# Optimization experiments

Measured on AMD Instinct MI355X. Metric: run time of the kernel, lower is better.

The kernel has to match this reference:

```python
import jax, jax.numpy as jnp
import numpy as np
from jax.scipy.stats import norm

N_TOK, D_MODEL, N_EXP, N_SEL = 16384, 4096, 16, 4
NOISE_EPS = 0.01
LOSS_LAMBDA = 0.01


def setup_inputs() -> dict:
    key = jax.random.key(0)
    kx, k1, k2, kn, kz = jax.random.split(key, 5)
    x = jax.random.normal(kx, (N_TOK, D_MODEL), dtype=jnp.float32)
    w1 = jax.random.normal(k1, (N_EXP, D_MODEL), dtype=jnp.float32) * 0.02
    w2 = jax.random.normal(k2, (N_EXP, N_EXP), dtype=jnp.float32) * 0.02
    wn = jax.random.normal(kn, (N_EXP, D_MODEL), dtype=jnp.float32) * 0.02
    noise = jax.random.normal(kz, (N_TOK, N_EXP), dtype=jnp.float32)
    return {"x": x, "w1": w1, "w2": w2, "wn": wn, "noise": noise}


def _cv_squared(v, eps=1e-10):
    # torch .var() is unbiased (ddof=1)
    return jnp.var(v, ddof=1) / (jnp.mean(v) ** 2 + eps)


def reference(x, w1, w2, wn, noise):
    # MLP gate: Linear(D->E, no bias) -> tanh -> Linear(E->E, no bias)
    logits_gate = jnp.einsum("te,fe->tf", jnp.tanh(jnp.einsum("td,ed->te", x, w1)), w2)
    noise_control = jax.nn.softplus(jnp.einsum("td,ed->te", x, wn)) + NOISE_EPS
    logits_noise = noise * noise_control
    logits = logits_gate + logits_noise  # [T, E]

    m = min(N_SEL + 1, N_EXP)  # k+1 values for threshold computation
    top_logits, top_indices = jax.lax.top_k(logits, m)  # [T, m]
    top_k_logits = top_logits[:, :N_SEL]
    top_k_indices = top_indices[:, :N_SEL]
    top_k_scores = jax.nn.softmax(top_k_logits, axis=1)  # [T, k]

    # importance: scatter top-k scores back to dense [T, E]
    rows = jnp.arange(N_TOK)[:, None]
    scores_filtered = jnp.zeros_like(logits).at[rows, top_k_indices].set(top_k_scores)
    importance = scores_filtered.sum(0)  # [E]

    # load: smooth estimator via Normal CDF (faithful to source, which
    # compares logits_noise against the in/out thresholds)
    threshold_if_in = top_logits[:, N_SEL:N_SEL + 1]       # (k+1)-th top value, [T,1]
    threshold_if_out = top_logits[:, N_SEL - 1:N_SEL]      # k-th top value, [T,1]
    is_in = logits_noise > threshold_if_in
    prob_if_in = norm.cdf((logits_gate - threshold_if_in) / noise_control)
    prob_if_out = norm.cdf((logits_gate - threshold_if_out) / noise_control)
    prob = jnp.where(is_in, prob_if_in, prob_if_out)
    load = prob.sum(0)  # [E]

    gate_loss = LOSS_LAMBDA * (_cv_squared(importance) + _cv_squared(load))
    return top_k_indices, top_k_scores, gate_loss
```

## Files before the change

### kernel.cpp

```cpp
#include <hip/hip_runtime.h>
#include <math.h>

#define N_TOK   16384
#define D_MODEL 4096
#define N_EXP   16
#define N_SEL   4
#define WELEM   (N_EXP * D_MODEL)
#define TILES   4

typedef __bf16 bf16x8 __attribute__((ext_vector_type(8)));
typedef float  f32x4  __attribute__((ext_vector_type(4)));

#define MFMA(a, b, c) __builtin_amdgcn_mfma_f32_16x16x32_bf16((a), (b), (c), 0, 0, 0)

__global__ __launch_bounds__(256) void wprep_kernel(const float* __restrict__ w1,
                                                    const float* __restrict__ wn,
                                                    __bf16* __restrict__ wbuf,
                                                    float* __restrict__ g_acc)
{
    const int i = blockIdx.x * 256 + threadIdx.x;
    if (blockIdx.x == 0 && threadIdx.x < 2 * N_EXP) g_acc[threadIdx.x] = 0.f;
    {
        const float v = w1[i];
        const __bf16 h = (__bf16)v;  const float r1 = v - (float)h;
        const __bf16 m = (__bf16)r1; const float r2 = r1 - (float)m;
        wbuf[i] = h; wbuf[WELEM + i] = m; wbuf[2 * WELEM + i] = (__bf16)r2;
    }
    {
        const float v = wn[i];
        const __bf16 h = (__bf16)v;  const float r1 = v - (float)h;
        const __bf16 m = (__bf16)r1; const float r2 = r1 - (float)m;
        wbuf[3 * WELEM + i] = h; wbuf[4 * WELEM + i] = m; wbuf[5 * WELEM + i] = (__bf16)r2;
    }
}

__device__ __forceinline__ void split8(const float4 a, const float4 b,
                                       bf16x8& h, bf16x8& m, bf16x8& l)
{
    const float v[8] = {a.x, a.y, a.z, a.w, b.x, b.y, b.z, b.w};
    #pragma unroll
    for (int j = 0; j < 8; ++j) {
        const float vv = v[j];
        const __bf16 hh = (__bf16)vv;  const float r1 = vv - (float)hh;
        const __bf16 mm = (__bf16)r1;  const float r2 = r1 - (float)mm;
        h[j] = hh; m[j] = mm; l[j] = (__bf16)r2;
    }
}

__global__ __launch_bounds__(512, 4) void gate_kernel(
    const float* __restrict__ x, const __bf16* __restrict__ wbuf,
    const float* __restrict__ w2, const float* __restrict__ noise,
    float* __restrict__ out, float* __restrict__ g_imp, float* __restrict__ g_load)
{
    __shared__ float red[8][TILES][16][33];
    __shared__ float dsum[TILES][16][33];
    __shared__ float s_imp[N_EXP], s_ld[N_EXP];

    const int tid  = threadIdx.x;
    const int lane = tid & 63;
    const int wv   = tid >> 6;
    const int ml   = lane & 15;
    const int q    = lane >> 4;
    const int t0   = blockIdx.x * (TILES * 16);

    const __bf16* w1h = wbuf;
    const __bf16* w1m = wbuf + WELEM;
    const __bf16* w1l = wbuf + 2 * WELEM;
    const __bf16* wnh = wbuf + 3 * WELEM;
    const __bf16* wnm = wbuf + 4 * WELEM;
    const __bf16* wnl = wbuf + 5 * WELEM;

    const size_t xoff0 = (size_t)(t0 + ml) * D_MODEL + wv * 512 + q * 8;
    const int    woff  = ml * D_MODEL + wv * 512 + q * 8;

    f32x4 c1[TILES], c2[TILES];
    #pragma unroll
    for (int tt = 0; tt < TILES; ++tt) {
        c1[tt] = (f32x4){0.f, 0.f, 0.f, 0.f};
        c2[tt] = (f32x4){0.f, 0.f, 0.f, 0.f};
    }

    #pragma unroll 2
    for (int it = 0; it < 16; ++it) {
        const int ko = it * 32;
        const bf16x8 a1h = *(const bf16x8*)(w1h + woff + ko);
        const bf16x8 a1m = *(const bf16x8*)(w1m + woff + ko);
        const bf16x8 a1l = *(const bf16x8*)(w1l + woff + ko);
        const bf16x8 a2h = *(const bf16x8*)(wnh + woff + ko);
        const bf16x8 a2m = *(const bf16x8*)(wnm + woff + ko);
        const bf16x8 a2l = *(const bf16x8*)(wnl + woff + ko);
        float4 xa[TILES], xb[TILES];
        #pragma unroll
        for (int tt = 0; tt < TILES; ++tt) {
            const size_t xo = xoff0 + (size_t)(16 * tt) * D_MODEL + ko;
            xa[tt] = *(const float4*)(x + xo);
            xb[tt] = *(const float4*)(x + xo + 4);
        }

        #pragma unroll
        for (int tt = 0; tt < TILES; ++tt) {
            bf16x8 xh, xm8, xl;
            split8(xa[tt], xb[tt], xh, xm8, xl);
            c1[tt] = MFMA(a1h, xh, c1[tt]);   c2[tt] = MFMA(a2h, xh, c2[tt]);
            c1[tt] = MFMA(a1h, xm8, c1[tt]);  c2[tt] = MFMA(a2h, xm8, c2[tt]);
            c1[tt] = MFMA(a1m, xh, c1[tt]);   c2[tt] = MFMA(a2m, xh, c2[tt]);
            c1[tt] = MFMA(a1h, xl, c1[tt]);   c2[tt] = MFMA(a2h, xl, c2[tt]);
            c1[tt] = MFMA(a1l, xh, c1[tt]);   c2[tt] = MFMA(a2l, xh, c2[tt]);
            c1[tt] = MFMA(a1m, xm8, c1[tt]);  c2[tt] = MFMA(a2m, xm8, c2[tt]);
        }
    }

    #pragma unroll
    for (int tt = 0; tt < TILES; ++tt) {
        #pragma unroll
        for (int r = 0; r < 4; ++r) {
            red[wv][tt][ml][q * 4 + r]      = c1[tt][r];
            red[wv][tt][ml][16 + q * 4 + r] = c2[tt][r];
        }
    }
    __syncthreads();

    for (int idx = tid; idx < TILES * 512; idx += 512) {
        const int tt = idx >> 9, tk = (idx >> 5) & 15, o = idx & 31;
        float s = 0.f;
        #pragma unroll
        for (int w = 0; w < 8; ++w) s += red[w][tt][tk][o];
        dsum[tt][tk][o] = s;
    }
    if (tid < N_EXP) { s_imp[tid] = 0.f; s_ld[tid] = 0.f; }
    __syncthreads();

    if (tid < TILES * 16) {
        const int tt = tid >> 4, tk = tid & 15;
        const int t = t0 + tid;
        float dot[32];
        #pragma unroll
        for (int e = 0; e < 32; ++e) dot[e] = dsum[tt][tk][e];

        float th[N_EXP], nc[N_EXP];
        #pragma unroll
        for (int e = 0; e < N_EXP; ++e) th[e] = tanhf(dot[e]);
        #pragma unroll
        for (int e = 0; e < N_EXP; ++e) {
            const float v = dot[N_EXP + e];
            nc[e] = fmaxf(v, 0.f) + log1pf(expf(-fabsf(v))) + 0.01f;
        }

        float lg[N_EXP];
        #pragma unroll
        for (int f = 0; f < N_EXP; ++f) {
            float s = 0.f;
            #pragma unroll
            for (int e = 0; e < N_EXP; ++e) s = fmaf(th[e], w2[f * 16 + e], s);
            lg[f] = s;
        }

        float ln[N_EXP], v[N_EXP];
        {
            const float4* nz = (const float4*)(noise + (size_t)t * 16);
            const float4 n0 = nz[0], n1 = nz[1], n2 = nz[2], n3 = nz[3];
            const float nzv[16] = {n0.x, n0.y, n0.z, n0.w, n1.x, n1.y, n1.z, n1.w,
                                   n2.x, n2.y, n2.z, n2.w, n3.x, n3.y, n3.z, n3.w};
            #pragma unroll
            for (int e = 0; e < N_EXP; ++e) {
                ln[e] = nzv[e] * nc[e];
                v[e]  = lg[e] + ln[e];
            }
        }

        float tv[5]; int ti[5];
        #pragma unroll
        for (int j = 0; j < 5; ++j) {
            float best = -INFINITY; int bi = 0;
            #pragma unroll
            for (int e = 0; e < N_EXP; ++e) {
                bool taken = false;
                #pragma unroll
                for (int jj = 0; jj < 5; ++jj)
                    if (jj < j) taken = taken || (ti[jj] == e);
                if (!taken && v[e] > best) { best = v[e]; bi = e; }
            }
            tv[j] = best; ti[j] = bi;
        }

        const float mx = tv[0];
        float ex[4], ssum = 0.f;
        #pragma unroll
        for (int j = 0; j < 4; ++j) { ex[j] = expf(tv[j] - mx); ssum += ex[j]; }
        const float inv = 1.f / ssum;
        float sc[4];
        #pragma unroll
        for (int j = 0; j < 4; ++j) sc[j] = ex[j] * inv;

        #pragma unroll
        for (int j = 0; j < 4; ++j) atomicAdd(&s_imp[ti[j]], sc[j]);

        const float thr_in = tv[4], thr_out = tv[3];
        #pragma unroll
        for (int e = 0; e < N_EXP; ++e) {
            const bool  is_in = ln[e] > thr_in;
            const float thr   = is_in ? thr_in : thr_out;
            const float z     = (lg[e] - thr) / nc[e];
            const float prob  = 0.5f * (1.f + erff(z * 0.70710678118654752f));
            atomicAdd(&s_ld[e], prob);
        }

        ((float4*)out)[t] = make_float4((float)ti[0], (float)ti[1],
                                        (float)ti[2], (float)ti[3]);
        ((float4*)(out + N_TOK * N_SEL))[t] = make_float4(sc[0], sc[1], sc[2], sc[3]);
    }
    __syncthreads();
    if (tid < N_EXP)            atomicAdd(&g_imp[tid], s_imp[tid]);
    else if (tid < 2 * N_EXP)   atomicAdd(&g_load[tid - N_EXP], s_ld[tid - N_EXP]);
}

__global__ void loss_kernel(const float* __restrict__ g_imp,
                            const float* __restrict__ g_load,
                            float* __restrict__ out)
{
    if (threadIdx.x == 0 && blockIdx.x == 0) {
        double mi = 0.0, ml = 0.0;
        for (int e = 0; e < N_EXP; ++e) { mi += g_imp[e]; ml += g_load[e]; }
        mi /= N_EXP; ml /= N_EXP;
        double vi = 0.0, vl = 0.0;
        for (int e = 0; e < N_EXP; ++e) {
            const double di = g_imp[e] - mi;  vi += di * di;
            const double dl = g_load[e] - ml; vl += dl * dl;
        }
        vi /= (N_EXP - 1); vl /= (N_EXP - 1);
        const double ci = vi / (mi * mi + 1e-10);
        const double cl = vl / (ml * ml + 1e-10);
        out[N_TOK * N_SEL * 2] = (float)(0.01 * (ci + cl));
    }
}

extern "C" void kernel_launch(void* const* d_in, const int* in_sizes, int n_in,
                              void* d_out, int out_size, void* d_ws, size_t ws_size,
                              hipStream_t stream)
{
    const float* x     = (const float*)d_in[0];
    const float* w1    = (const float*)d_in[1];
    const float* w2    = (const float*)d_in[2];
    const float* wn    = (const float*)d_in[3];
    const float* noise = (const float*)d_in[4];
    float* out = (float*)d_out;

    __bf16* wbuf  = (__bf16*)d_ws;
    float*  g_imp = (float*)((char*)d_ws + (1 << 20));
    float*  g_load = g_imp + N_EXP;

    wprep_kernel<<<WELEM / 256, 256, 0, stream>>>(w1, wn, wbuf, g_imp);
    gate_kernel<<<N_TOK / (TILES * 16), 512, 0, stream>>>(x, wbuf, w2, noise, out,
                                                          g_imp, g_load);
    loss_kernel<<<1, 64, 0, stream>>>(g_imp, g_load, out);
}
```

Baseline: 415.7 us.

## Stage x tiles through double-buffered LDS with coalesced loads, halve tokens per block

Token tiles per block drop from 4 to 2 (32 tokens per block, twice as many blocks). Each K step now loads x with fully coalesced float4 global reads into one of two LDS buffers, prefetching the next step while MFMAs run on the current one. This is meant to fix the strided per-lane global access pattern and overlap memory latency with compute. It adds a __syncthreads per step and LDS traffic, and the smaller tile means the weight splits are reloaded per fewer tokens.

```diff
diff --git a/kernel.cpp b/kernel.cpp
--- a/kernel.cpp
+++ b/kernel.cpp
@@ -6,7 +6,7 @@
 #define N_EXP   16
 #define N_SEL   4
 #define WELEM   (N_EXP * D_MODEL)
-#define TILES   4
+#define TILES   2
 
 typedef __bf16 bf16x8 __attribute__((ext_vector_type(8)));
 typedef float  f32x4  __attribute__((ext_vector_type(4)));
@@ -52,8 +52,7 @@
     const float* __restrict__ w2, const float* __restrict__ noise,
     float* __restrict__ out, float* __restrict__ g_imp, float* __restrict__ g_load)
 {
-    __shared__ float red[8][TILES][16][33];
-    __shared__ float dsum[TILES][16][33];
+    __shared__ float smem[2][8 * 32 * 33];
     __shared__ float s_imp[N_EXP], s_ld[N_EXP];
 
     const int tid  = threadIdx.x;
@@ -70,8 +69,23 @@
     const __bf16* wnm = wbuf + 4 * WELEM;
     const __bf16* wnl = wbuf + 5 * WELEM;
 
-    const size_t xoff0 = (size_t)(t0 + ml) * D_MODEL + wv * 512 + q * 8;
-    const int    woff  = ml * D_MODEL + wv * 512 + q * 8;
+    const int woff = ml * D_MODEL + wv * 512 + q * 8;
+
+    int gb0, gb1, gb2, gb3, lb0, lb1, lb2, lb3;
+    {
+#define MAP(P, GB, LB)                                           \
+        {   const int fid  = (P) * 512 + tid;                    \
+            const int slot = fid & 7;                            \
+            const int s    = fid >> 3;                           \
+            const int r    = s >> 5;                             \
+            const int t    = s & 31;                             \
+            GB = (t0 + t) * D_MODEL + r * 512 + slot * 4;        \
+            LB = (r * 32 + t) * 33 + slot * 4;  }
+        MAP(0, gb0, lb0) MAP(1, gb1, lb1) MAP(2, gb2, lb2) MAP(3, gb3, lb3)
+#undef MAP
+    }
+    const int lr0 = (wv * 32 + ml) * 33 + q * 8;
+    const int lr1 = lr0 + 16 * 33;
 
     f32x4 c1[TILES], c2[TILES];
     #pragma unroll
@@ -80,42 +94,82 @@
         c2[tt] = (f32x4){0.f, 0.f, 0.f, 0.f};
     }
 
-    #pragma unroll 2
-    for (int it = 0; it < 16; ++it) {
-        const int ko = it * 32;
-        const bf16x8 a1h = *(const bf16x8*)(w1h + woff + ko);
-        const bf16x8 a1m = *(const bf16x8*)(w1m + woff + ko);
-        const bf16x8 a1l = *(const bf16x8*)(w1l + woff + ko);
-        const bf16x8 a2h = *(const bf16x8*)(wnh + woff + ko);
-        const bf16x8 a2m = *(const bf16x8*)(wnm + woff + ko);
-        const bf16x8 a2l = *(const bf16x8*)(wnl + woff + ko);
-        float4 xa[TILES], xb[TILES];
-        #pragma unroll
-        for (int tt = 0; tt < TILES; ++tt) {
-            const size_t xo = xoff0 + (size_t)(16 * tt) * D_MODEL + ko;
-            xa[tt] = *(const float4*)(x + xo);
-            xb[tt] = *(const float4*)(x + xo + 4);
-        }
-
-        #pragma unroll
-        for (int tt = 0; tt < TILES; ++tt) {
-            bf16x8 xh, xm8, xl;
-            split8(xa[tt], xb[tt], xh, xm8, xl);
-            c1[tt] = MFMA(a1h, xh, c1[tt]);   c2[tt] = MFMA(a2h, xh, c2[tt]);
-            c1[tt] = MFMA(a1h, xm8, c1[tt]);  c2[tt] = MFMA(a2h, xm8, c2[tt]);
-            c1[tt] = MFMA(a1m, xh, c1[tt]);   c2[tt] = MFMA(a2m, xh, c2[tt]);
-            c1[tt] = MFMA(a1h, xl, c1[tt]);   c2[tt] = MFMA(a2h, xl, c2[tt]);
-            c1[tt] = MFMA(a1l, xh, c1[tt]);   c2[tt] = MFMA(a2l, xh, c2[tt]);
-            c1[tt] = MFMA(a1m, xm8, c1[tt]);  c2[tt] = MFMA(a2m, xm8, c2[tt]);
-        }
-    }
+    float* bufA = smem[0];
+    float* bufB = smem[1];
+
+    {
+        const float4 s0 = *(const float4*)(x + gb0);
+        const float4 s1 = *(const float4*)(x + gb1);
+        const float4 s2 = *(const float4*)(x + gb2);
+        const float4 s3 = *(const float4*)(x + gb3);
+        *(float4*)(bufA + lb0) = s0;
+        *(float4*)(bufA + lb1) = s1;
+        *(float4*)(bufA + lb2) = s2;
+        *(float4*)(bufA + lb3) = s3;
+        __syncthreads();
+    }
+
+#define STEP(CUR, NXT, IT)                                                    \
+    {                                                                          \
+        const int ko = (IT) * 32;                                              \
+        const bf16x8 a1h = *(const bf16x8*)(w1h + woff + ko);                  \
+        const bf16x8 a1m = *(const bf16x8*)(w1m + woff + ko);                  \
+        const bf16x8 a1l = *(const bf16x8*)(w1l + woff + ko);                  \
+        const bf16x8 a2h = *(const bf16x8*)(wnh + woff + ko);                  \
+        const bf16x8 a2m = *(const bf16x8*)(wnm + woff + ko);                  \
+        const bf16x8 a2l = *(const bf16x8*)(wnl + woff + ko);                  \
+        float4 sg0, sg1, sg2, sg3;                                             \
+        if ((IT) < 15) {                                                       \
+            const int co = ((IT) + 1) * 32;                                    \
+            sg0 = *(const float4*)(x + gb0 + co);                              \
+            sg1 = *(const float4*)(x + gb1 + co);                              \
+            sg2 = *(const float4*)(x + gb2 + co);                              \
+            sg3 = *(const float4*)(x + gb3 + co);                              \
+        }                                                                      \
+        const float4 xa0 = *(const float4*)((CUR) + lr0);                      \
+        const float4 xb0 = *(const float4*)((CUR) + lr0 + 4);                  \
+        const float4 xa1 = *(const float4*)((CUR) + lr1);                      \
+        const float4 xb1 = *(const float4*)((CUR) + lr1 + 4);                  \
+        bf16x8 xh0, xm0, xl0, xh1, xm1, xl1;                                   \
+        split8(xa0, xb0, xh0, xm0, xl0);                                       \
+        split8(xa1, xb1, xh1, xm1, xl1);                                       \
+        c1[0] = MFMA(a1h, xh0, c1[0]);  c2[0] = MFMA(a2h, xh0, c2[0]);         \
+        c1[1] = MFMA(a1h, xh1, c1[1]);  c2[1] = MFMA(a2h, xh1, c2[1]);         \
+        c1[0] = MFMA(a1h, xm0, c1[0]);  c2[0] = MFMA(a2h, xm0, c2[0]);         \
+        c1[1] = MFMA(a1h, xm1, c1[1]);  c2[1] = MFMA(a2h, xm1, c2[1]);         \
+        c1[0] = MFMA(a1m, xh0, c1[0]);  c2[0] = MFMA(a2m, xh0, c2[0]);         \
+        c1[1] = MFMA(a1m, xh1, c1[1]);  c2[1] = MFMA(a2m, xh1, c2[1]);         \
+        c1[0] = MFMA(a1h, xl0, c1[0]);  c2[0] = MFMA(a2h, xl0, c2[0]);         \
+        c1[1] = MFMA(a1h, xl1, c1[1]);  c2[1] = MFMA(a2h, xl1, c2[1]);         \
+        c1[0] = MFMA(a1l, xh0, c1[0]);  c2[0] = MFMA(a2l, xh0, c2[0]);         \
+        c1[1] = MFMA(a1l, xh1, c1[1]);  c2[1] = MFMA(a2l, xh1, c2[1]);         \
+        c1[0] = MFMA(a1m, xm0, c1[0]);  c2[0] = MFMA(a2m, xm0, c2[0]);         \
+        c1[1] = MFMA(a1m, xm1, c1[1]);  c2[1] = MFMA(a2m, xm1, c2[1]);         \
+        if ((IT) < 15) {                                                       \
+            *(float4*)((NXT) + lb0) = sg0;                                     \
+            *(float4*)((NXT) + lb1) = sg1;                                     \
+            *(float4*)((NXT) + lb2) = sg2;                                     \
+            *(float4*)((NXT) + lb3) = sg3;                                     \
+        }                                                                      \
+        __syncthreads();                                                       \
+    }
+
+    #pragma unroll
+    for (int ith = 0; ith < 8; ++ith) {
+        STEP(bufA, bufB, 2 * ith)
+        STEP(bufB, bufA, 2 * ith + 1)
+    }
+#undef STEP
+
+    float* red  = smem[0];
+    float* dsum = smem[1];
 
     #pragma unroll
     for (int tt = 0; tt < TILES; ++tt) {
         #pragma unroll
         for (int r = 0; r < 4; ++r) {
-            red[wv][tt][ml][q * 4 + r]      = c1[tt][r];
-            red[wv][tt][ml][16 + q * 4 + r] = c2[tt][r];
+            red[((wv * TILES + tt) * 16 + ml) * 33 + q * 4 + r]      = c1[tt][r];
+            red[((wv * TILES + tt) * 16 + ml) * 33 + 16 + q * 4 + r] = c2[tt][r];
         }
     }
     __syncthreads();
@@ -124,8 +178,8 @@
         const int tt = idx >> 9, tk = (idx >> 5) & 15, o = idx & 31;
         float s = 0.f;
         #pragma unroll
-        for (int w = 0; w < 8; ++w) s += red[w][tt][tk][o];
-        dsum[tt][tk][o] = s;
+        for (int w = 0; w < 8; ++w) s += red[((w * TILES + tt) * 16 + tk) * 33 + o];
+        dsum[(tt * 16 + tk) * 33 + o] = s;
     }
     if (tid < N_EXP) { s_imp[tid] = 0.f; s_ld[tid] = 0.f; }
     __syncthreads();
@@ -135,7 +189,7 @@
         const int t = t0 + tid;
         float dot[32];
         #pragma unroll
-        for (int e = 0; e < 32; ++e) dot[e] = dsum[tt][tk][e];
+        for (int e = 0; e < 32; ++e) dot[e] = dsum[(tt * 16 + tk) * 33 + e];
 
         float th[N_EXP], nc[N_EXP];
         #pragma unroll
```

New measurement: 405.7 us. 1.02x faster.
